# Optimization experiments

Hardware: AMD Instinct MI355X
Metric: run time of the kernel (lower is better)

## Reference

```python
import jax, jax.numpy as jnp
import numpy as np

N_NODES = 50000
N_EDGES = 800000
IN_DIM = 128
HID = 128
HEADS = 4
OUT_DIM = 32
NEG_SLOPE = 0.2  # DGL GATConv default


def _gat_params(key, in_dim, out_feat, heads):
    k1, k2, k3 = jax.random.split(key, 3)
    s = 1.0 / np.sqrt(in_dim)
    W = jax.random.normal(k1, (in_dim, heads * out_feat), jnp.float32) * s
    attn_l = jax.random.normal(k2, (heads, out_feat), jnp.float32) * 0.1
    attn_r = jax.random.normal(k3, (heads, out_feat), jnp.float32) * 0.1
    b = jnp.zeros((heads * out_feat,), jnp.float32)
    return W, attn_l, attn_r, b


def setup_inputs() -> dict:
    key = jax.random.key(0)
    ks = jax.random.split(key, 10)
    inp = {
        "x_am": jax.random.normal(ks[0], (N_NODES, IN_DIM), jnp.float32),
        "x_ph": jax.random.normal(ks[1], (N_NODES, IN_DIM), jnp.float32),
        "exist": jax.random.uniform(ks[2], (N_EDGES,), jnp.float32),
        "am_exist": jax.random.uniform(ks[3], (N_EDGES,), jnp.float32),
        "src": jax.random.randint(ks[4], (N_EDGES,), 0, N_NODES, jnp.int32),
        "dst": jax.random.randint(ks[5], (N_EDGES,), 0, N_NODES, jnp.int32),
    }
    # layer 0 (input_dim -> hidden//head per head), layer 1 (hidden -> output_dim per head)
    inp["W0a"], inp["al0a"], inp["ar0a"], inp["b0a"] = _gat_params(ks[6], IN_DIM, HID // HEADS, HEADS)
    inp["W0p"], inp["al0p"], inp["ar0p"], inp["b0p"] = _gat_params(ks[7], IN_DIM, HID // HEADS, HEADS)
    inp["W1a"], inp["al1a"], inp["ar1a"], inp["b1a"] = _gat_params(ks[8], HID, OUT_DIM, HEADS)
    inp["W1p"], inp["al1p"], inp["ar1p"], inp["b1p"] = _gat_params(ks[9], HID, OUT_DIM, HEADS)
    return inp


def gat_conv(x, src, dst, W, attn_l, attn_r, b, edge_w, n_nodes):
    """DGL-style GATConv with edge_weight: out[i] = sum_{e: dst=i} softmax_i(LeakyReLU(el[src]+er[dst])) * w_e * ft[src]."""
    heads, outf = attn_l.shape
    ft = (x @ W).reshape(-1, heads, outf)                 # (N, H, F)
    el = jnp.sum(ft * attn_l, axis=-1)                    # (N, H)
    er = jnp.sum(ft * attn_r, axis=-1)                    # (N, H)
    e = jax.nn.leaky_relu(el[src] + er[dst], NEG_SLOPE)   # (E, H)
    emax = jax.ops.segment_max(e, dst, num_segments=n_nodes)
    emax = jnp.where(jnp.isfinite(emax), emax, 0.0)       # guard isolated nodes
    ex = jnp.exp(e - emax[dst])
    denom = jax.ops.segment_sum(ex, dst, num_segments=n_nodes)
    a = ex / jnp.maximum(denom[dst], 1e-9)                # edge softmax over incoming edges
    a = a * edge_w[:, None]                               # post-softmax edge weighting
    out = jax.ops.segment_sum(ft[src] * a[:, :, None], dst, num_segments=n_nodes)  # (N, H, F)
    return out + b.reshape(heads, outf)


def reference(x_am, x_ph, exist, am_exist,
              W0a, al0a, ar0a, b0a, W0p, al0p, ar0p, b0p,
              W1a, al1a, ar1a, b1a, W1p, al1p, ar1p, b1p,
              src, dst):
    n = x_am.shape[0]
    # layer 0: GATConv -> flatten -> ReLU (dropout rate 0 in eval)
    h_am = gat_conv(x_am, src, dst, W0a, al0a, ar0a, b0a, am_exist, n)
    h_ph = gat_conv(x_ph, src, dst, W0p, al0p, ar0p, b0p, exist, n)
    h_am = jax.nn.relu(h_am.reshape(n, -1))
    h_ph = jax.nn.relu(h_ph.reshape(n, -1))
    # layer 1 (last): GATConv -> mean over heads
    h_am = gat_conv(h_am, src, dst, W1a, al1a, ar1a, b1a, am_exist, n).mean(axis=1)
    h_ph = gat_conv(h_ph, src, dst, W1p, al1p, ar1p, b1p, exist, n).mean(axis=1)
    return (h_am, h_ph)
```

## Files before the change

### kernel.cpp

```cpp
#include <hip/hip_runtime.h>
#include <hip/hip_fp16.h>


typedef _Float16 f16x8 __attribute__((ext_vector_type(8)));
typedef float f32x4 __attribute__((ext_vector_type(4)));

struct GemmP { const void* X; const __half* Wt; const float *al, *ar; __half* Y; float *el, *er; };
struct ChP   { const __half* ft; const float* X; const float* bias; void* out; };
struct CoefP { const float *el, *er; float* X; };

__global__ void hist_kernel(const int* __restrict__ dst, int* __restrict__ counts, int E) {
  int e = blockIdx.x * blockDim.x + threadIdx.x;
  if (e < E) atomicAdd(&counts[dst[e]], 1);
}

__global__ __launch_bounds__(256) void scan1_kernel(const int* __restrict__ counts,
                                                    int* __restrict__ incl,
                                                    int* __restrict__ bsum, int n) {
  __shared__ int lds[256];
  int i = blockIdx.x * 256 + threadIdx.x;
  int v = (i < n) ? counts[i] : 0;
  lds[threadIdx.x] = v;
  __syncthreads();
  for (int off = 1; off < 256; off <<= 1) {
    int t = (threadIdx.x >= off) ? lds[threadIdx.x - off] : 0;
    __syncthreads();
    lds[threadIdx.x] += t;
    __syncthreads();
  }
  if (i < n) incl[i] = lds[threadIdx.x];
  if (threadIdx.x == 255) bsum[blockIdx.x] = lds[255];
}

__global__ __launch_bounds__(256) void scan2_kernel(int* __restrict__ bsum, int nb) {
  __shared__ int lds[256];
  int carry = 0;
  for (int base = 0; base < nb; base += 256) {
    int i = base + threadIdx.x;
    int v = (i < nb) ? bsum[i] : 0;
    lds[threadIdx.x] = v;
    __syncthreads();
    for (int off = 1; off < 256; off <<= 1) {
      int t = (threadIdx.x >= off) ? lds[threadIdx.x - off] : 0;
      __syncthreads();
      lds[threadIdx.x] += t;
      __syncthreads();
    }
    if (i < nb) bsum[i] = carry + lds[threadIdx.x] - v;
    carry += lds[255];
    __syncthreads();
  }
}

__global__ void scan3_kernel(const int* __restrict__ counts, const int* __restrict__ incl,
                             const int* __restrict__ bsum_ex, int* __restrict__ offsets,
                             int* __restrict__ cursor, int n, int E) {
  int i = blockIdx.x * blockDim.x + threadIdx.x;
  if (i < n) {
    int v = incl[i] - counts[i] + bsum_ex[i >> 8];
    offsets[i] = v;
    cursor[i] = v;
  }
  if (i == 0) offsets[n] = E;
}

__global__ void fill_kernel(const int* __restrict__ src, const int* __restrict__ dst,
                            const float* __restrict__ exist, const float* __restrict__ am_exist,
                            int* __restrict__ cursor, int4* __restrict__ edge16, int E) {
  int e = blockIdx.x * blockDim.x + threadIdx.x;
  if (e >= E) return;
  int d = dst[e];
  int pos = atomicAdd(&cursor[d], 1);
  edge16[pos] = make_int4(src[e], d, __float_as_int(am_exist[e]), __float_as_int(exist[e]));
}

__global__ void wprep_kernel(const float* __restrict__ W0a, const float* __restrict__ W0p,
                             const float* __restrict__ W1a, const float* __restrict__ W1p,
                             __half* __restrict__ Wt) {
  int m = blockIdx.y;
  const float* W = (m == 0) ? W0a : (m == 1) ? W0p : (m == 2) ? W1a : W1p;
  __half* O = Wt + (size_t)m * 16384;
  int i = blockIdx.x * 256 + threadIdx.x;
  int nn = i >> 7, k = i & 127;
  O[nn * 128 + k] = __float2half_rn(W[k * 128 + nn]);
}

template <int AFP16>
__global__ __launch_bounds__(256) void gemm_kernel(GemmP p0, GemmP p1, int n) {
  GemmP p = blockIdx.y ? p1 : p0;
  constexpr int LDH = 72;
  constexpr int LDE = 136;
  __shared__ __half lds[2 * 128 * LDH];
  __half* As = lds;
  __half* Ws = lds + 128 * LDH;
  int t = threadIdx.x;
  int row0 = blockIdx.x << 7;
  int wv = t >> 6, lane = t & 63;
  int m = lane & 15, q = lane >> 4;

  f32x4 acc[2][8];
#pragma unroll
  for (int rt = 0; rt < 2; ++rt)
#pragma unroll
    for (int ct = 0; ct < 8; ++ct) acc[rt][ct] = (f32x4){0.f, 0.f, 0.f, 0.f};

#pragma unroll
  for (int kh = 0; kh < 2; ++kh) {
    __syncthreads();
    if (AFP16) {
      const __half* Xh = (const __half*)p.X;
#pragma unroll
      for (int i = 0; i < 4; ++i) {
        int c = t + (i << 8);
        int r = c >> 3, o8 = c & 7;
        uint4 v = make_uint4(0, 0, 0, 0);
        if (row0 + r < n)
          v = *(const uint4*)(Xh + (size_t)(row0 + r) * 128 + (kh << 6) + (o8 << 3));
        *(uint4*)(As + r * LDH + (o8 << 3)) = v;
      }
    } else {
      const float* Xf = (const float*)p.X;
#pragma unroll
      for (int i = 0; i < 8; ++i) {
        int c = t + (i << 8);
        int r = c >> 4, f4 = c & 15;
        float4 v = make_float4(0.f, 0.f, 0.f, 0.f);
        if (row0 + r < n)
          v = *(const float4*)(Xf + (size_t)(row0 + r) * 128 + (kh << 6) + (f4 << 2));
        union { __half h[4]; uint2 u; } pk;
        pk.h[0] = __float2half_rn(v.x); pk.h[1] = __float2half_rn(v.y);
        pk.h[2] = __float2half_rn(v.z); pk.h[3] = __float2half_rn(v.w);
        *(uint2*)(As + r * LDH + (f4 << 2)) = pk.u;
      }
    }
#pragma unroll
    for (int i = 0; i < 4; ++i) {
      int c = t + (i << 8);
      int r = c >> 3, o8 = c & 7;
      uint4 v = *(const uint4*)(p.Wt + (size_t)r * 128 + (kh << 6) + (o8 << 3));
      *(uint4*)(Ws + r * LDH + (o8 << 3)) = v;
    }
    __syncthreads();
#pragma unroll
    for (int kc = 0; kc < 2; ++kc) {
      f16x8 a0 = *(const f16x8*)(As + (wv * 32 + m) * LDH + kc * 32 + q * 8);
      f16x8 a1 = *(const f16x8*)(As + (wv * 32 + 16 + m) * LDH + kc * 32 + q * 8);
#pragma unroll
      for (int ct = 0; ct < 8; ++ct) {
        f16x8 b = *(const f16x8*)(Ws + (ct * 16 + m) * LDH + kc * 32 + q * 8);
        acc[0][ct] = __builtin_amdgcn_mfma_f32_16x16x32_f16(a0, b, acc[0][ct], 0, 0, 0);
        acc[1][ct] = __builtin_amdgcn_mfma_f32_16x16x32_f16(a1, b, acc[1][ct], 0, 0, 0);
      }
    }
  }
  __syncthreads();
#pragma unroll
  for (int rt = 0; rt < 2; ++rt) {
    int rbase = wv * 32 + rt * 16 + q * 4;
#pragma unroll
    for (int ct = 0; ct < 8; ++ct) {
      int col = ct * 16 + m;
#pragma unroll
      for (int r = 0; r < 4; ++r)
        lds[(rbase + r) * LDE + col] = __float2half_rn(acc[rt][ct][r]);
    }
  }
  __syncthreads();
  {
    int r = t & 127;
    int half = t >> 7;
    int row = row0 + r;
    if (row < n) {
      float e0 = 0.f, e1 = 0.f, r0 = 0.f, r1 = 0.f;
#pragma unroll
      for (int i = 0; i < 8; ++i) {
        int cbase = half * 64 + i * 8;
        f16x8 v = *(const f16x8*)(lds + r * LDE + cbase);
        *(uint4*)(p.Y + (size_t)row * 128 + cbase) = *(const uint4*)&v;
#pragma unroll
        for (int j = 0; j < 8; ++j) {
          float f = (float)v[j];
          float av = p.al[cbase + j];
          float rv = p.ar[cbase + j];
          if (((i * 8 + j) >> 5) == 0) { e0 = fmaf(f, av, e0); r0 = fmaf(f, rv, r0); }
          else                         { e1 = fmaf(f, av, e1); r1 = fmaf(f, rv, r1); }
        }
      }
      *(float2*)(p.el + (size_t)row * 4 + half * 2) = make_float2(e0, e1);
      *(float2*)(p.er + (size_t)row * 4 + half * 2) = make_float2(r0, r1);
    }
  }
}

__global__ __launch_bounds__(256) void coef_kernel(CoefP a, CoefP b,
                                                   const int4* __restrict__ edge16, int E) {
  int e = blockIdx.x * 256 + threadIdx.x;
  if (e >= E) return;
  int4 r = edge16[e];
  int s = r.x, d = r.y;
  {
    float4 el = *(const float4*)(a.el + (size_t)s * 4);
    float4 er = *(const float4*)(a.er + (size_t)d * 4);
    float4 x;
    float v;
    v = el.x + er.x; v = (v > 0.f) ? v : 0.2f * v; x.x = __expf(v);
    v = el.y + er.y; v = (v > 0.f) ? v : 0.2f * v; x.y = __expf(v);
    v = el.z + er.z; v = (v > 0.f) ? v : 0.2f * v; x.z = __expf(v);
    v = el.w + er.w; v = (v > 0.f) ? v : 0.2f * v; x.w = __expf(v);
    *(float4*)(a.X + (size_t)e * 4) = x;
  }
  {
    float4 el = *(const float4*)(b.el + (size_t)s * 4);
    float4 er = *(const float4*)(b.er + (size_t)d * 4);
    float4 x;
    float v;
    v = el.x + er.x; v = (v > 0.f) ? v : 0.2f * v; x.x = __expf(v);
    v = el.y + er.y; v = (v > 0.f) ? v : 0.2f * v; x.y = __expf(v);
    v = el.z + er.z; v = (v > 0.f) ? v : 0.2f * v; x.z = __expf(v);
    v = el.w + er.w; v = (v > 0.f) ? v : 0.2f * v; x.w = __expf(v);
    *(float4*)(b.X + (size_t)e * 4) = x;
  }
}

template <int LAYER>
__global__ __launch_bounds__(256) void gather_kernel(ChP c0, ChP c1,
                                                     const int* __restrict__ offs,
                                                     const int4* __restrict__ edge16, int n) {
  int t = threadIdx.x;
  int w = t >> 6;
  int lane = t & 63;
  int node = blockIdx.x * 2 + (w >> 1);
  int ch = w & 1;
  if (node >= n) return;
  ChP P = ch ? c1 : c0;
  int hh = lane >> 4;

  int start = __builtin_amdgcn_readfirstlane(offs[node]);
  int end = __builtin_amdgcn_readfirstlane(offs[node + 1]);
  const __half2* ftbase = (const __half2*)P.ft;
  const float* Xb = P.X;

  float acc0 = 0.f, acc1 = 0.f, l = 0.f;
  int k = start;
  while (k + 8 <= end) {
    int4 ed[8];
#pragma unroll
    for (int j = 0; j < 8; ++j) ed[j] = edge16[k + j];
    const float* Xk = Xb + (size_t)k * 4;
    float xs[8];
#pragma unroll
    for (int j = 0; j < 8; ++j) xs[j] = Xk[j * 4 + hh];
#pragma unroll
    for (int j = 0; j < 8; ++j) {
      int s = ed[j].x;
      float wgt = __int_as_float(ch ? ed[j].w : ed[j].z);
      __half2 fh = ftbase[(size_t)s * 64 + lane];
      float x = xs[j];
      l += x;
      float cv = x * wgt;
      acc0 = fmaf(cv, __low2float(fh), acc0);
      acc1 = fmaf(cv, __high2float(fh), acc1);
    }
    k += 8;
  }
  for (; k < end; ++k) {
    int4 ed = edge16[k];
    int s = ed.x;
    float wgt = __int_as_float(ch ? ed.w : ed.z);
    float x = Xb[(size_t)k * 4 + hh];
    __half2 fh = ftbase[(size_t)s * 64 + lane];
    l += x;
    float cv = x * wgt;
    acc0 = fmaf(cv, __low2float(fh), acc0);
    acc1 = fmaf(cv, __high2float(fh), acc1);
  }

  float rl = 1.f / fmaxf(l, 1e-9f);
  float2 b2 = *(const float2*)(P.bias + lane * 2);
  float v0 = fmaf(acc0, rl, b2.x);
  float v1 = fmaf(acc1, rl, b2.y);
  if (LAYER == 0) {
    __half2 h = __floats2half2_rn(fmaxf(v0, 0.f), fmaxf(v1, 0.f));
    ((__half2*)P.out)[(size_t)node * 64 + lane] = h;
  } else {
    v0 += __shfl_xor(v0, 16); v1 += __shfl_xor(v1, 16);
    v0 += __shfl_xor(v0, 32); v1 += __shfl_xor(v1, 32);
    if (lane < 16) {
      *(float2*)((float*)P.out + (size_t)node * 32 + lane * 2) =
          make_float2(0.25f * v0, 0.25f * v1);
    }
  }
}

extern "C" void kernel_launch(void* const* d_in, const int* in_sizes, int n_in,
                              void* d_out, int out_size, void* d_ws, size_t ws_size,
                              hipStream_t stream) {
  const float* x_am = (const float*)d_in[0];
  const float* x_ph = (const float*)d_in[1];
  const float* exist = (const float*)d_in[2];
  const float* am_exist = (const float*)d_in[3];
  const int* src = (const int*)d_in[4];
  const int* dst = (const int*)d_in[5];
  const float* W0a = (const float*)d_in[6];
  const float* al0a = (const float*)d_in[7];
  const float* ar0a = (const float*)d_in[8];
  const float* b0a = (const float*)d_in[9];
  const float* W0p = (const float*)d_in[10];
  const float* al0p = (const float*)d_in[11];
  const float* ar0p = (const float*)d_in[12];
  const float* b0p = (const float*)d_in[13];
  const float* W1a = (const float*)d_in[14];
  const float* al1a = (const float*)d_in[15];
  const float* ar1a = (const float*)d_in[16];
  const float* b1a = (const float*)d_in[17];
  const float* W1p = (const float*)d_in[18];
  const float* al1p = (const float*)d_in[19];
  const float* ar1p = (const float*)d_in[20];
  const float* b1p = (const float*)d_in[21];

  int n = in_sizes[0] / 128;
  int E = in_sizes[2];
  int N_pad = (n + 255) & ~255;
  int nb = (n + 255) / 256;
  int NB_pad = (nb + 63) & ~63;

  size_t szN = (size_t)N_pad * 4;
  size_t szOffs = (size_t)(N_pad + 8) * 4;
  size_t szE16 = (size_t)E * 16;
  size_t szFt16 = (size_t)n * 128 * 2;
  size_t szEl = (size_t)N_pad * 4 * 4;
  size_t szWt = (size_t)4 * 128 * 128 * 2;
  size_t szX = (size_t)E * 16;

  auto rnd = [](size_t b) { return (b + 255) & ~(size_t)255; };
  size_t fixed = 3 * rnd(szN) + rnd((size_t)NB_pad * 4) + rnd(szOffs) + rnd(szE16) +
                 4 * rnd(szEl) + rnd(szWt) + rnd(szX);
  bool dual = ws_size >= fixed + 4 * rnd(szFt16) + rnd(szX);

  char* p = (char*)d_ws;
  auto take = [&](size_t b) { char* q = p; p += (b + 255) & ~(size_t)255; return q; };
  int* counts = (int*)take(szN);
  int* cursor = (int*)take(szN);
  int* incl = (int*)take(szN);
  int* bsum = (int*)take((size_t)NB_pad * 4);
  int* offs = (int*)take(szOffs);
  int4* edge16 = (int4*)take(szE16);
  __half* Wt = (__half*)take(szWt);
  float* el_am = (float*)take(szEl);
  float* el_ph = (float*)take(szEl);
  float* er_am = (float*)take(szEl);
  float* er_ph = (float*)take(szEl);
  float* X_am = (float*)take(szX);
  float* X_ph = dual ? (float*)take(szX) : X_am;
  __half* ft_am = (__half*)take(szFt16);
  __half* ft_ph = dual ? (__half*)take(szFt16) : ft_am;
  __half* hb_am = (__half*)take(szFt16);
  __half* hb_ph = dual ? (__half*)take(szFt16) : hb_am;

  float* out_am = (float*)d_out;
  float* out_ph = out_am + (size_t)n * 32;

  hipMemsetAsync(counts, 0, szN, stream);
  hist_kernel<<<(E + 255) / 256, 256, 0, stream>>>(dst, counts, E);
  wprep_kernel<<<dim3(64, 4), 256, 0, stream>>>(W0a, W0p, W1a, W1p, Wt);
  scan1_kernel<<<nb, 256, 0, stream>>>(counts, incl, bsum, n);
  scan2_kernel<<<1, 256, 0, stream>>>(bsum, nb);
  scan3_kernel<<<nb, 256, 0, stream>>>(counts, incl, bsum, offs, cursor, n, E);
  fill_kernel<<<(E + 255) / 256, 256, 0, stream>>>(src, dst, exist, am_exist,
                                                   cursor, edge16, E);

  int gg = (n + 127) / 128;
  int gw = (n + 1) / 2;
  int ce = (E + 255) / 256;
  GemmP g0a{x_am, Wt,          al0a, ar0a, ft_am, el_am, er_am};
  GemmP g0p{x_ph, Wt + 16384,  al0p, ar0p, ft_ph, el_ph, er_ph};
  GemmP g1a{hb_am, Wt + 32768, al1a, ar1a, ft_am, el_am, er_am};
  GemmP g1p{hb_ph, Wt + 49152, al1p, ar1p, ft_ph, el_ph, er_ph};
  CoefP ka{el_am, er_am, X_am};
  CoefP kp{el_ph, er_ph, X_ph};
  ChP c0a{ft_am, X_am, b0a, hb_am};
  ChP c0p{ft_ph, X_ph, b0p, hb_ph};
  ChP c1a{ft_am, X_am, b1a, out_am};
  ChP c1p{ft_ph, X_ph, b1p, out_ph};

  if (dual) {
    gemm_kernel<0><<<dim3(gg, 2), 256, 0, stream>>>(g0a, g0p, n);
    coef_kernel<<<ce, 256, 0, stream>>>(ka, kp, edge16, E);
    gather_kernel<0><<<gw, 256, 0, stream>>>(c0a, c0p, offs, edge16, n);
    gemm_kernel<1><<<dim3(gg, 2), 256, 0, stream>>>(g1a, g1p, n);
    coef_kernel<<<ce, 256, 0, stream>>>(ka, kp, edge16, E);
    gather_kernel<1><<<gw, 256, 0, stream>>>(c1a, c1p, offs, edge16, n);
  } else {
    gemm_kernel<0><<<dim3(gg, 2), 256, 0, stream>>>(g0a, g0a, n);
    coef_kernel<<<ce, 256, 0, stream>>>(ka, ka, edge16, E);
    gather_kernel<0><<<gw, 256, 0, stream>>>(c0a, c0a, offs, edge16, n);
    gemm_kernel<1><<<dim3(gg, 2), 256, 0, stream>>>(g1a, g1a, n);
    coef_kernel<<<ce, 256, 0, stream>>>(ka, ka, edge16, E);
    gather_kernel<1><<<gw, 256, 0, stream>>>(c1a, c1a, offs, edge16, n);
    gemm_kernel<0><<<dim3(gg, 2), 256, 0, stream>>>(g0p, g0p, n);
    coef_kernel<<<ce, 256, 0, stream>>>(kp, kp, edge16, E);
    gather_kernel<0><<<gw, 256, 0, stream>>>(c0p, c0p, offs, edge16, n);
    gemm_kernel<1><<<dim3(gg, 2), 256, 0, stream>>>(g1p, g1p, n);
    coef_kernel<<<ce, 256, 0, stream>>>(kp, kp, edge16, E);
    gather_kernel<1><<<gw, 256, 0, stream>>>(c1p, c1p, offs, edge16, n);
  }
}
```

Baseline: 433.5 us.

## Fuse preprocessing launches, use decoupled-lookback scan, widen gather unroll

Merges the weight-transpose prep into the histogram kernel and replaces the three-kernel scan with a single-pass decoupled-lookback scan that uses atomic block IDs and spin-waiting on per-block state flags. This removes several small launches. The edge-record fill now uses non-temporal stores. The gather loop is unrolled to 16 edges, and the scalar tail is replaced by a clamped, masked 8-wide batch. These changes cut launch count and serial scan stages and raise memory-level parallelism in the gather. The trade-offs are more register pressure and a scan that depends on forward progress across blocks.

```diff
diff --git a/kernel.cpp b/kernel.cpp
--- a/kernel.cpp
+++ b/kernel.cpp
@@ -4,21 +4,40 @@
 
 typedef _Float16 f16x8 __attribute__((ext_vector_type(8)));
 typedef float f32x4 __attribute__((ext_vector_type(4)));
+typedef int i32x4 __attribute__((ext_vector_type(4)));
 
 struct GemmP { const void* X; const __half* Wt; const float *al, *ar; __half* Y; float *el, *er; };
 struct ChP   { const __half* ft; const float* X; const float* bias; void* out; };
 struct CoefP { const float *el, *er; float* X; };
 
-__global__ void hist_kernel(const int* __restrict__ dst, int* __restrict__ counts, int E) {
+__global__ void hist_wprep_kernel(const int* __restrict__ dst, int* __restrict__ counts, int E,
+                                  const float* __restrict__ W0a, const float* __restrict__ W0p,
+                                  const float* __restrict__ W1a, const float* __restrict__ W1p,
+                                  __half* __restrict__ Wt) {
   int e = blockIdx.x * blockDim.x + threadIdx.x;
   if (e < E) atomicAdd(&counts[dst[e]], 1);
-}
-
-__global__ __launch_bounds__(256) void scan1_kernel(const int* __restrict__ counts,
-                                                    int* __restrict__ incl,
-                                                    int* __restrict__ bsum, int n) {
+  if (e < 65536) {
+    int m = e >> 14, i = e & 16383;
+    const float* W = (m == 0) ? W0a : (m == 1) ? W0p : (m == 2) ? W1a : W1p;
+    int nn = i >> 7, k = i & 127;
+    Wt[(size_t)m * 16384 + nn * 128 + k] = __float2half_rn(W[k * 128 + nn]);
+  }
+}
+
+__global__ __launch_bounds__(256) void scan_kernel(const int* __restrict__ counts,
+                                                   int* __restrict__ offsets,
+                                                   int* __restrict__ cursor,
+                                                   int* __restrict__ sync,
+                                                   int nb_stride, int n, int E) {
   __shared__ int lds[256];
-  int i = blockIdx.x * 256 + threadIdx.x;
+  __shared__ int sbid, sprev;
+  int* state = sync + 64;
+  int* agg = state + nb_stride;
+  int* incl = agg + nb_stride;
+  if (threadIdx.x == 0) sbid = atomicAdd(sync, 1);
+  __syncthreads();
+  int bid = sbid;
+  int i = bid * 256 + threadIdx.x;
   int v = (i < n) ? counts[i] : 0;
   lds[threadIdx.x] = v;
   __syncthreads();
@@ -28,61 +47,52 @@
     lds[threadIdx.x] += t;
     __syncthreads();
   }
-  if (i < n) incl[i] = lds[threadIdx.x];
-  if (threadIdx.x == 255) bsum[blockIdx.x] = lds[255];
-}
-
-__global__ __launch_bounds__(256) void scan2_kernel(int* __restrict__ bsum, int nb) {
-  __shared__ int lds[256];
-  int carry = 0;
-  for (int base = 0; base < nb; base += 256) {
-    int i = base + threadIdx.x;
-    int v = (i < nb) ? bsum[i] : 0;
-    lds[threadIdx.x] = v;
-    __syncthreads();
-    for (int off = 1; off < 256; off <<= 1) {
-      int t = (threadIdx.x >= off) ? lds[threadIdx.x - off] : 0;
-      __syncthreads();
-      lds[threadIdx.x] += t;
-      __syncthreads();
-    }
-    if (i < nb) bsum[i] = carry + lds[threadIdx.x] - v;
-    carry += lds[255];
-    __syncthreads();
-  }
-}
-
-__global__ void scan3_kernel(const int* __restrict__ counts, const int* __restrict__ incl,
-                             const int* __restrict__ bsum_ex, int* __restrict__ offsets,
-                             int* __restrict__ cursor, int n, int E) {
-  int i = blockIdx.x * blockDim.x + threadIdx.x;
+  int total = lds[255];
+  if (threadIdx.x == 0) {
+    if (bid == 0) {
+      __hip_atomic_store(&incl[0], total, __ATOMIC_RELAXED, __HIP_MEMORY_SCOPE_AGENT);
+      __hip_atomic_store(&state[0], 2, __ATOMIC_RELEASE, __HIP_MEMORY_SCOPE_AGENT);
+      sprev = 0;
+    } else {
+      __hip_atomic_store(&agg[bid], total, __ATOMIC_RELAXED, __HIP_MEMORY_SCOPE_AGENT);
+      __hip_atomic_store(&state[bid], 1, __ATOMIC_RELEASE, __HIP_MEMORY_SCOPE_AGENT);
+      int run = 0, j = bid - 1;
+      while (true) {
+        int st;
+        do {
+          st = __hip_atomic_load(&state[j], __ATOMIC_ACQUIRE, __HIP_MEMORY_SCOPE_AGENT);
+        } while (st == 0);
+        if (st == 2) {
+          run += __hip_atomic_load(&incl[j], __ATOMIC_RELAXED, __HIP_MEMORY_SCOPE_AGENT);
+          break;
+        }
+        run += __hip_atomic_load(&agg[j], __ATOMIC_RELAXED, __HIP_MEMORY_SCOPE_AGENT);
+        --j;
+      }
+      __hip_atomic_store(&incl[bid], run + total, __ATOMIC_RELAXED, __HIP_MEMORY_SCOPE_AGENT);
+      __hip_atomic_store(&state[bid], 2, __ATOMIC_RELEASE, __HIP_MEMORY_SCOPE_AGENT);
+      sprev = run;
+    }
+  }
+  __syncthreads();
+  int prev = sprev;
   if (i < n) {
-    int v = incl[i] - counts[i] + bsum_ex[i >> 8];
-    offsets[i] = v;
-    cursor[i] = v;
+    int off = prev + lds[threadIdx.x] - v;
+    offsets[i] = off;
+    cursor[i] = off;
   }
   if (i == 0) offsets[n] = E;
 }
 
 __global__ void fill_kernel(const int* __restrict__ src, const int* __restrict__ dst,
                             const float* __restrict__ exist, const float* __restrict__ am_exist,
-                            int* __restrict__ cursor, int4* __restrict__ edge16, int E) {
+                            int* __restrict__ cursor, i32x4* __restrict__ edge16, int E) {
   int e = blockIdx.x * blockDim.x + threadIdx.x;
   if (e >= E) return;
   int d = dst[e];
   int pos = atomicAdd(&cursor[d], 1);
-  edge16[pos] = make_int4(src[e], d, __float_as_int(am_exist[e]), __float_as_int(exist[e]));
-}
-
-__global__ void wprep_kernel(const float* __restrict__ W0a, const float* __restrict__ W0p,
-                             const float* __restrict__ W1a, const float* __restrict__ W1p,
-                             __half* __restrict__ Wt) {
-  int m = blockIdx.y;
-  const float* W = (m == 0) ? W0a : (m == 1) ? W0p : (m == 2) ? W1a : W1p;
-  __half* O = Wt + (size_t)m * 16384;
-  int i = blockIdx.x * 256 + threadIdx.x;
-  int nn = i >> 7, k = i & 127;
-  O[nn * 128 + k] = __float2half_rn(W[k * 128 + nn]);
+  i32x4 rec = {src[e], d, __float_as_int(am_exist[e]), __float_as_int(exist[e])};
+  __builtin_nontemporal_store(rec, &edge16[pos]);
 }
 
 template <int AFP16>
@@ -242,14 +252,32 @@
 
   float acc0 = 0.f, acc1 = 0.f, l = 0.f;
   int k = start;
-  while (k + 8 <= end) {
+  for (; k + 16 <= end; k += 16) {
+    int4 ed[16];
+#pragma unroll
+    for (int j = 0; j < 16; ++j) ed[j] = edge16[k + j];
+    float xs[16];
+#pragma unroll
+    for (int j = 0; j < 16; ++j) xs[j] = Xb[(size_t)(k + j) * 4 + hh];
+#pragma unroll
+    for (int j = 0; j < 16; ++j) {
+      int s = ed[j].x;
+      float wgt = __int_as_float(ch ? ed[j].w : ed[j].z);
+      __half2 fh = ftbase[(size_t)s * 64 + lane];
+      float x = xs[j];
+      l += x;
+      float cv = x * wgt;
+      acc0 = fmaf(cv, __low2float(fh), acc0);
+      acc1 = fmaf(cv, __high2float(fh), acc1);
+    }
+  }
+  if (k + 8 <= end) {
     int4 ed[8];
 #pragma unroll
     for (int j = 0; j < 8; ++j) ed[j] = edge16[k + j];
-    const float* Xk = Xb + (size_t)k * 4;
     float xs[8];
 #pragma unroll
-    for (int j = 0; j < 8; ++j) xs[j] = Xk[j * 4 + hh];
+    for (int j = 0; j < 8; ++j) xs[j] = Xb[(size_t)(k + j) * 4 + hh];
 #pragma unroll
     for (int j = 0; j < 8; ++j) {
       int s = ed[j].x;
@@ -263,16 +291,29 @@
     }
     k += 8;
   }
-  for (; k < end; ++k) {
-    int4 ed = edge16[k];
-    int s = ed.x;
-    float wgt = __int_as_float(ch ? ed.w : ed.z);
-    float x = Xb[(size_t)k * 4 + hh];
-    __half2 fh = ftbase[(size_t)s * 64 + lane];
-    l += x;
-    float cv = x * wgt;
-    acc0 = fmaf(cv, __low2float(fh), acc0);
-    acc1 = fmaf(cv, __high2float(fh), acc1);
+  if (k < end) {
+    int4 ed[8];
+    int ci[8];
+#pragma unroll
+    for (int j = 0; j < 8; ++j) {
+      int idx = k + j;
+      ci[j] = (idx < end) ? idx : end - 1;
+      ed[j] = edge16[ci[j]];
+    }
+    float xs[8];
+#pragma unroll
+    for (int j = 0; j < 8; ++j) xs[j] = Xb[(size_t)ci[j] * 4 + hh];
+#pragma unroll
+    for (int j = 0; j < 8; ++j) {
+      int s = ed[j].x;
+      float wgt = __int_as_float(ch ? ed[j].w : ed[j].z);
+      __half2 fh = ftbase[(size_t)s * 64 + lane];
+      float x = (k + j < end) ? xs[j] : 0.f;
+      l += x;
+      float cv = x * wgt;
+      acc0 = fmaf(cv, __low2float(fh), acc0);
+      acc1 = fmaf(cv, __high2float(fh), acc1);
+    }
   }
 
   float rl = 1.f / fmaxf(l, 1e-9f);
@@ -325,6 +366,7 @@
   int NB_pad = (nb + 63) & ~63;
 
   size_t szN = (size_t)N_pad * 4;
+  size_t szSync = (size_t)(64 + 3 * NB_pad) * 4;
   size_t szOffs = (size_t)(N_pad + 8) * 4;
   size_t szE16 = (size_t)E * 16;
   size_t szFt16 = (size_t)n * 128 * 2;
@@ -333,18 +375,17 @@
   size_t szX = (size_t)E * 16;
 
   auto rnd = [](size_t b) { return (b + 255) & ~(size_t)255; };
-  size_t fixed = 3 * rnd(szN) + rnd((size_t)NB_pad * 4) + rnd(szOffs) + rnd(szE16) +
+  size_t fixed = 2 * rnd(szN) + rnd(szSync) + rnd(szOffs) + rnd(szE16) +
                  4 * rnd(szEl) + rnd(szWt) + rnd(szX);
   bool dual = ws_size >= fixed + 4 * rnd(szFt16) + rnd(szX);
 
   char* p = (char*)d_ws;
   auto take = [&](size_t b) { char* q = p; p += (b + 255) & ~(size_t)255; return q; };
   int* counts = (int*)take(szN);
+  int* sync = (int*)take(szSync);
   int* cursor = (int*)take(szN);
-  int* incl = (int*)take(szN);
-  int* bsum = (int*)take((size_t)NB_pad * 4);
   int* offs = (int*)take(szOffs);
-  int4* edge16 = (int4*)take(szE16);
+  i32x4* edge16 = (i32x4*)take(szE16);
   __half* Wt = (__half*)take(szWt);
   float* el_am = (float*)take(szEl);
   float* el_ph = (float*)take(szEl);
@@ -360,18 +401,17 @@
   float* out_am = (float*)d_out;
   float* out_ph = out_am + (size_t)n * 32;
 
-  hipMemsetAsync(counts, 0, szN, stream);
-  hist_kernel<<<(E + 255) / 256, 256, 0, stream>>>(dst, counts, E);
-  wprep_kernel<<<dim3(64, 4), 256, 0, stream>>>(W0a, W0p, W1a, W1p, Wt);
-  scan1_kernel<<<nb, 256, 0, stream>>>(counts, incl, bsum, n);
-  scan2_kernel<<<1, 256, 0, stream>>>(bsum, nb);
-  scan3_kernel<<<nb, 256, 0, stream>>>(counts, incl, bsum, offs, cursor, n, E);
+  (void)hipMemsetAsync(counts, 0, rnd(szN) + rnd(szSync), stream);
+  hist_wprep_kernel<<<(E + 255) / 256, 256, 0, stream>>>(dst, counts, E,
+                                                         W0a, W0p, W1a, W1p, Wt);
+  scan_kernel<<<nb, 256, 0, stream>>>(counts, offs, cursor, sync, NB_pad, n, E);
   fill_kernel<<<(E + 255) / 256, 256, 0, stream>>>(src, dst, exist, am_exist,
                                                    cursor, edge16, E);
 
   int gg = (n + 127) / 128;
   int gw = (n + 1) / 2;
   int ce = (E + 255) / 256;
+  const int4* edge16c = (const int4*)edge16;
   GemmP g0a{x_am, Wt,          al0a, ar0a, ft_am, el_am, er_am};
   GemmP g0p{x_ph, Wt + 16384,  al0p, ar0p, ft_ph, el_ph, er_ph};
   GemmP g1a{hb_am, Wt + 32768, al1a, ar1a, ft_am, el_am, er_am};
@@ -385,23 +425,23 @@
 
   if (dual) {
     gemm_kernel<0><<<dim3(gg, 2), 256, 0, stream>>>(g0a, g0p, n);
-    coef_kernel<<<ce, 256, 0, stream>>>(ka, kp, edge16, E);
-    gather_kernel<0><<<gw, 256, 0, stream>>>(c0a, c0p, offs, edge16, n);
+    coef_kernel<<<ce, 256, 0, stream>>>(ka, kp, edge16c, E);
+    gather_kernel<0><<<gw, 256, 0, stream>>>(c0a, c0p, offs, edge16c, n);
     gemm_kernel<1><<<dim3(gg, 2), 256, 0, stream>>>(g1a, g1p, n);
-    coef_kernel<<<ce, 256, 0, stream>>>(ka, kp, edge16, E);
-    gather_kernel<1><<<gw, 256, 0, stream>>>(c1a, c1p, offs, edge16, n);
+    coef_kernel<<<ce, 256, 0, stream>>>(ka, kp, edge16c, E);
+    gather_kernel<1><<<gw, 256, 0, stream>>>(c1a, c1p, offs, edge16c, n);
   } else {
     gemm_kernel<0><<<dim3(gg, 2), 256, 0, stream>>>(g0a, g0a, n);
-    coef_kernel<<<ce, 256, 0, stream>>>(ka, ka, edge16, E);
-    gather_kernel<0><<<gw, 256, 0, stream>>>(c0a, c0a, offs, edge16, n);
+    coef_kernel<<<ce, 256, 0, stream>>>(ka, ka, edge16c, E);
+    gather_kernel<0><<<gw, 256, 0, stream>>>(c0a, c0a, offs, edge16c, n);
     gemm_kernel<1><<<dim3(gg, 2), 256, 0, stream>>>(g1a, g1a, n);
-    coef_kernel<<<ce, 256, 0, stream>>>(ka, ka, edge16, E);
-    gather_kernel<1><<<gw, 256, 0, stream>>>(c1a, c1a, offs, edge16, n);
+    coef_kernel<<<ce, 256, 0, stream>>>(ka, ka, edge16c, E);
+    gather_kernel<1><<<gw, 256, 0, stream>>>(c1a, c1a, offs, edge16c, n);
     gemm_kernel<0><<<dim3(gg, 2), 256, 0, stream>>>(g0p, g0p, n);
-    coef_kernel<<<ce, 256, 0, stream>>>(kp, kp, edge16, E);
-    gather_kernel<0><<<gw, 256, 0, stream>>>(c0p, c0p, offs, edge16, n);
+    coef_kernel<<<ce, 256, 0, stream>>>(kp, kp, edge16c, E);
+    gather_kernel<0><<<gw, 256, 0, stream>>>(c0p, c0p, offs, edge16c, n);
     gemm_kernel<1><<<dim3(gg, 2), 256, 0, stream>>>(g1p, g1p, n);
-    coef_kernel<<<ce, 256, 0, stream>>>(kp, kp, edge16, E);
-    gather_kernel<1><<<gw, 256, 0, stream>>>(c1p, c1p, offs, edge16, n);
-  }
-}
+    coef_kernel<<<ce, 256, 0, stream>>>(kp, kp, edge16c, E);
+    gather_kernel<1><<<gw, 256, 0, stream>>>(c1p, c1p, offs, edge16c, n);
+  }
+}
```

New measurement: 479.9 us. 10.7% more time.
